# Kernel optimization log

Hardware: AMD Instinct MI355X
Metric: run time of the kernel (lower is better)

Reference implementation:

```python
import jax, jax.numpy as jnp
import numpy as np

HEADS = 12
DIM = 64
NEG = 1e12


def _rope(x, sin, cos):
    # x: [B,T,H,d]; sin/cos: [T,d] (interleaved, each freq repeated twice)
    x2 = jnp.stack([-x[..., 1::2], x[..., ::2]], axis=-1).reshape(x.shape)
    return x * cos[None, :, None, :] + x2 * sin[None, :, None, :]


def setup_inputs() -> dict:
    key = jax.random.key(0)
    k1, k2 = jax.random.split(key, 2)
    hidden_states = jax.random.normal(k1, (8, 1024, 768), dtype=jnp.float32)
    attention_mask = jnp.ones((8, 1024), dtype=jnp.int32)
    W = jax.random.normal(k2, (768, HEADS * DIM * 2), dtype=jnp.float32) * 0.02
    b = jnp.zeros((HEADS * DIM * 2,), dtype=jnp.float32)
    return {"hidden_states": hidden_states, "attention_mask": attention_mask, "W": W, "b": b}


def reference(hidden_states, attention_mask, W, b):
    B, T, D = hidden_states.shape
    H, d = HEADS, DIM
    proj = hidden_states @ W + b                      # [B,T,2*H*d]
    proj = proj.reshape(B, T, H, 2 * d)
    qw, kw = proj[..., :d], proj[..., d:]             # [B,T,H,d] each

    # sinusoidal interleaved RoPE tables
    pos = jnp.arange(T, dtype=jnp.float32)[:, None]                     # [T,1]
    inv_freq = jnp.power(10000.0, -2.0 * jnp.arange(d // 2, dtype=jnp.float32) / d)
    ang = pos * inv_freq                                                # [T,d/2]
    sin = jnp.repeat(jnp.sin(ang), 2, axis=-1)                          # [T,d]
    cos = jnp.repeat(jnp.cos(ang), 2, axis=-1)                          # [T,d]

    qw = _rope(qw, sin, cos)
    kw = _rope(kw, sin, cos)

    logits = jnp.einsum('bmhd,bnhd->bhmn', qw, kw)    # [B,H,T,T]

    # pad mask along key axis (matches torch expand of [B,1,1,T])
    m = attention_mask.astype(logits.dtype)[:, None, None, :]
    logits = logits * m - (1.0 - m) * NEG

    # strict lower-triangular mask (spans with start > end)
    tri = jnp.tril(jnp.ones((T, T), dtype=logits.dtype), -1)
    logits = logits - tri * NEG

    return logits / (d ** 0.5)
```

## Files before the change

kernel.cpp:

```cpp
#include <hip/hip_runtime.h>

#define NEG 1000000000000.0f

typedef __attribute__((ext_vector_type(4))) float f32x4;
typedef __attribute__((ext_vector_type(8))) short bf16x8;

__device__ __forceinline__ unsigned short f2bf(float f) {
    union { float f; unsigned u; } a;
    a.f = f;
    unsigned u = a.u;
    return (unsigned short)((u + 0x7FFFu + ((u >> 16) & 1u)) >> 16);
}

__device__ __forceinline__ void gload_lds16(const void* g, void* l) {
    __builtin_amdgcn_global_load_lds(
        (const __attribute__((address_space(1))) unsigned int*)g,
        (__attribute__((address_space(3))) unsigned int*)l, 16, 0, 0);
}

__global__ void cvt_bf16_kernel(const float* __restrict__ in,
                                unsigned short* __restrict__ out, int n4) {
    int i = blockIdx.x * blockDim.x + threadIdx.x;
    if (i < n4) {
        float4 v = ((const float4*)in)[i];
        ushort4 o;
        o.x = f2bf(v.x); o.y = f2bf(v.y); o.z = f2bf(v.z); o.w = f2bf(v.w);
        ((ushort4*)out)[i] = o;
    }
}

__global__ void transpose_w_kernel(const float* __restrict__ W,
                                   unsigned short* __restrict__ Wt) {
    __shared__ float tile[32][33];
    int n0 = blockIdx.x * 32, k0 = blockIdx.y * 32;
    int tx = threadIdx.x & 31, ty = threadIdx.x >> 5;
    #pragma unroll
    for (int r = 0; r < 32; r += 8)
        tile[ty + r][tx] = W[(k0 + ty + r) * 1536 + n0 + tx];
    __syncthreads();
    #pragma unroll
    for (int r = 0; r < 32; r += 8)
        Wt[(n0 + ty + r) * 768 + k0 + tx] = f2bf(tile[tx][ty + r]);
}

__global__ void rope_table_kernel(float* __restrict__ cosT, float* __restrict__ sinT) {
    int idx = blockIdx.x * blockDim.x + threadIdx.x;
    int t = idx >> 5, i = idx & 31;
    float inv = powf(10000.0f, -(float)i / 32.0f);
    float ang = (float)t * inv;
    cosT[idx] = cosf(ang);
    sinT[idx] = sinf(ang);
}

__global__ __launch_bounds__(256) void proj_rope_kernel(
    const unsigned short* __restrict__ A,
    const unsigned short* __restrict__ Bt,
    const float* __restrict__ bias,
    const float* __restrict__ cosT, const float* __restrict__ sinT,
    unsigned short* __restrict__ qout, unsigned short* __restrict__ kout)
{
    __shared__ unsigned short As[128 * 64];
    __shared__ unsigned short Bs[128 * 64];
    const int tid = threadIdx.x;
    const int lane = tid & 63, w = tid >> 6;
    const int wm = w >> 1, wn = w & 1;
    const int bm = blockIdx.y * 128, bn = blockIdx.x * 128;
    const int l15 = lane & 15, l4 = lane >> 4;

    int crow[4], gcol[4], lbase[4];
    #pragma unroll
    for (int i = 0; i < 4; ++i) {
        int c = i * 256 + w * 64 + lane;
        crow[i] = c >> 3;
        gcol[i] = ((c & 7) ^ (crow[i] & 7)) * 8;
        lbase[i] = (i * 256 + w * 64) * 8;
    }

    f32x4 acc[4][4] = {};
    const int swr = l15 & 7;

    for (int k0 = 0; k0 < 768; k0 += 64) {
        __syncthreads();
        #pragma unroll
        for (int i = 0; i < 4; ++i) {
            gload_lds16(&A[(size_t)(bm + crow[i]) * 768 + k0 + gcol[i]], &As[lbase[i]]);
            gload_lds16(&Bt[(size_t)(bn + crow[i]) * 768 + k0 + gcol[i]], &Bs[lbase[i]]);
        }
        __syncthreads();
        #pragma unroll
        for (int ks = 0; ks < 2; ++ks) {
            bf16x8 af[4], bq[4];
            #pragma unroll
            for (int i = 0; i < 4; ++i) {
                const int ar = wm * 64 + i * 16 + l15;
                const int br = wn * 64 + i * 16 + l15;
                const int cc = (ks * 4 + l4) ^ swr;
                af[i] = *(const bf16x8*)&As[(ar * 8 + cc) * 8];
                bq[i] = *(const bf16x8*)&Bs[(br * 8 + cc) * 8];
            }
            #pragma unroll
            for (int i = 0; i < 4; ++i)
                #pragma unroll
                for (int j = 0; j < 4; ++j)
                    acc[i][j] = __builtin_amdgcn_mfma_f32_16x16x32_bf16(
                        af[i], bq[j], acc[i][j], 0, 0, 0);
        }
    }

    const int rbase = bm + wm * 64 + l4 * 4;
    const int cbase = bn + wn * 64 + l15;
    #pragma unroll
    for (int mi = 0; mi < 4; ++mi) {
        #pragma unroll
        for (int ni = 0; ni < 4; ++ni) {
            const int n = cbase + ni * 16;
            const float bv = bias[n];
            const int h = n >> 7, ww = n & 127;
            const int d = ww & 63, fi = d >> 1;
            unsigned short* __restrict__ dst = (ww < 64) ? qout : kout;
            #pragma unroll
            for (int j = 0; j < 4; ++j) {
                const int m = rbase + mi * 16 + j;
                const int t = m & 1023, bb = m >> 10;
                float v = acc[mi][ni][j] + bv;
                float p = __shfl_xor(v, 1, 64);
                float c = cosT[t * 32 + fi], s = sinT[t * 32 + fi];
                float r = (d & 1) ? fmaf(v, c, p * s) : fmaf(v, c, -p * s);
                dst[((bb * 12 + h) * 1024 + t) * 64 + d] = f2bf(r);
            }
        }
    }
}

__global__ __launch_bounds__(256) void logits_kernel(
    const unsigned short* __restrict__ q, const unsigned short* __restrict__ k,
    const int* __restrict__ mask, float* __restrict__ out)
{
    const int tid = threadIdx.x;
    const int tn = blockIdx.x, tm = blockIdx.y, z = blockIdx.z;
    const int bb = z / 12;

    if (tn < tm) {
        const int c4 = (tid & 31) * 4;
        const int r0 = tid >> 5;
        const int nb = tn * 128 + c4;
        float4 v;
        #pragma unroll
        for (int e = 0; e < 4; ++e) {
            float mv = (float)mask[bb * 1024 + nb + e];
            float addc = -(1.0f - mv) * NEG;
            ((float*)&v)[e] = (addc - NEG) * 0.125f;
        }
        float* __restrict__ base = out + (size_t)(z * 1024 + tm * 128) * 1024 + nb;
        #pragma unroll
        for (int r = 0; r < 16; ++r)
            *(float4*)&base[(size_t)(r * 8 + r0) * 1024] = v;
        return;
    }

    __shared__ float tr[4][16][68];
    const int lane = tid & 63, w = tid >> 6;
    const int wm = w >> 1, wn = w & 1;
    const int l15 = lane & 15, l4 = lane >> 4;

    f32x4 acc[4][4] = {};
    const unsigned short* __restrict__ qb = q + (size_t)(z * 1024 + tm * 128) * 64;
    const unsigned short* __restrict__ kb = k + (size_t)(z * 1024 + tn * 128) * 64;

    #pragma unroll
    for (int ks = 0; ks < 2; ++ks) {
        bf16x8 af[4], bq[4];
        #pragma unroll
        for (int i = 0; i < 4; ++i) {
            af[i] = *(const bf16x8*)&qb[(size_t)(wm * 64 + i * 16 + l15) * 64 + ks * 32 + l4 * 8];
            bq[i] = *(const bf16x8*)&kb[(size_t)(wn * 64 + i * 16 + l15) * 64 + ks * 32 + l4 * 8];
        }
        #pragma unroll
        for (int i = 0; i < 4; ++i)
            #pragma unroll
            for (int j = 0; j < 4; ++j)
                acc[i][j] = __builtin_amdgcn_mfma_f32_16x16x32_bf16(
                    af[i], bq[j], acc[i][j], 0, 0, 0);
    }

    const int rw = tm * 128 + wm * 64;
    const int cw = tn * 128 + wn * 64;
    float mv[4], addc[4];
    int ncol[4];
    #pragma unroll
    for (int ni = 0; ni < 4; ++ni) {
        ncol[ni] = cw + ni * 16 + l15;
        mv[ni] = (float)mask[bb * 1024 + ncol[ni]];
        addc[ni] = -(1.0f - mv[ni]) * NEG;
    }
    float* __restrict__ outz = out + (size_t)z * 1024 * 1024;
    #pragma unroll
    for (int mi = 0; mi < 4; ++mi) {
        #pragma unroll
        for (int ni = 0; ni < 4; ++ni)
            #pragma unroll
            for (int j = 0; j < 4; ++j) {
                const int m = rw + mi * 16 + l4 * 4 + j;
                float s = acc[mi][ni][j];
                tr[w][l4 * 4 + j][ni * 16 + l15] =
                    (s * mv[ni] + addc[ni] - (ncol[ni] < m ? NEG : 0.0f)) * 0.125f;
            }
        __syncthreads();
        #pragma unroll
        for (int ri = 0; ri < 4; ++ri) {
            float4 vv = *(const float4*)&tr[w][ri * 4 + l4][l15 * 4];
            *(float4*)&outz[(size_t)(rw + mi * 16 + ri * 4 + l4) * 1024 + cw + l15 * 4] = vv;
        }
        __syncthreads();
    }
}

extern "C" void kernel_launch(void* const* d_in, const int* in_sizes, int n_in,
                              void* d_out, int out_size, void* d_ws, size_t ws_size,
                              hipStream_t stream) {
    const float* hs   = (const float*)d_in[0];
    const int*   mask = (const int*)d_in[1];
    const float* W    = (const float*)d_in[2];
    const float* bias = (const float*)d_in[3];
    float* out = (float*)d_out;

    char* ws = (char*)d_ws;
    unsigned short* qbuf = (unsigned short*)(ws + 0);
    unsigned short* kbuf = (unsigned short*)(ws + 12582912);
    unsigned short* hsb  = (unsigned short*)(ws + 25165824);
    unsigned short* wtb  = (unsigned short*)(ws + 37748736);
    float* cosT = (float*)(ws + 40108032);
    float* sinT = (float*)(ws + 40239104);

    cvt_bf16_kernel<<<6291456 / 4 / 256, 256, 0, stream>>>(hs, hsb, 6291456 / 4);
    transpose_w_kernel<<<dim3(48, 24), 256, 0, stream>>>(W, wtb);
    rope_table_kernel<<<128, 256, 0, stream>>>(cosT, sinT);
    proj_rope_kernel<<<dim3(12, 64), 256, 0, stream>>>(hsb, wtb, bias, cosT, sinT,
                                                       qbuf, kbuf);
    logits_kernel<<<dim3(8, 8, 96), 256, 0, stream>>>(qbuf, kbuf, mask, out);
}
```

Baseline: 501.4 us.

## Stage projection epilogue through LDS for vectorized RoPE stores; use wave-local fences

The projection epilogue now writes each wave's accumulator tile to a per-wave LDS buffer. It then reads rows back so each lane applies RoPE to 8 contiguous dims, using float4 cos/sin loads and a single 16-byte bf16 store, replacing the scattered 2-byte stores and shuffles. In both kernels the block-wide __syncthreads around per-wave transpose buffers is replaced by an lgkmcnt wait plus a sched barrier, since each wave only touches its own slice. This relies on wave-local LDS visibility being guaranteed by the waitcnt alone.

```diff
diff --git a/kernel.cpp b/kernel.cpp
--- a/kernel.cpp
+++ b/kernel.cpp
@@ -4,6 +4,7 @@
 
 typedef __attribute__((ext_vector_type(4))) float f32x4;
 typedef __attribute__((ext_vector_type(8))) short bf16x8;
+typedef __attribute__((ext_vector_type(8))) unsigned short u16x8;
 
 __device__ __forceinline__ unsigned short f2bf(float f) {
     union { float f; unsigned u; } a;
@@ -16,6 +17,11 @@
     __builtin_amdgcn_global_load_lds(
         (const __attribute__((address_space(1))) unsigned int*)g,
         (__attribute__((address_space(3))) unsigned int*)l, 16, 0, 0);
+}
+
+__device__ __forceinline__ void lds_fence() {
+    asm volatile("s_waitcnt lgkmcnt(0)" ::: "memory");
+    __builtin_amdgcn_sched_barrier(0);
 }
 
 __global__ void cvt_bf16_kernel(const float* __restrict__ in,
@@ -61,6 +67,7 @@
 {
     __shared__ unsigned short As[128 * 64];
     __shared__ unsigned short Bs[128 * 64];
+    __shared__ float trp[4][16][68];
     const int tid = threadIdx.x;
     const int lane = tid & 63, w = tid >> 6;
     const int wm = w >> 1, wn = w & 1;
@@ -107,28 +114,44 @@
         }
     }
 
-    const int rbase = bm + wm * 64 + l4 * 4;
-    const int cbase = bn + wn * 64 + l15;
+    const int h = blockIdx.x;
+    const int bbq = bm >> 10;
+    const int tbase = bm & 1023;
+    unsigned short* __restrict__ dstb =
+        ((wn == 0) ? qout : kout) + (size_t)(bbq * 12 + h) * 1024 * 64;
+    float bv[4];
+    #pragma unroll
+    for (int ni = 0; ni < 4; ++ni) bv[ni] = bias[bn + wn * 64 + ni * 16 + l15];
+
     #pragma unroll
     for (int mi = 0; mi < 4; ++mi) {
         #pragma unroll
-        for (int ni = 0; ni < 4; ++ni) {
-            const int n = cbase + ni * 16;
-            const float bv = bias[n];
-            const int h = n >> 7, ww = n & 127;
-            const int d = ww & 63, fi = d >> 1;
-            unsigned short* __restrict__ dst = (ww < 64) ? qout : kout;
-            #pragma unroll
-            for (int j = 0; j < 4; ++j) {
-                const int m = rbase + mi * 16 + j;
-                const int t = m & 1023, bb = m >> 10;
-                float v = acc[mi][ni][j] + bv;
-                float p = __shfl_xor(v, 1, 64);
-                float c = cosT[t * 32 + fi], s = sinT[t * 32 + fi];
-                float r = (d & 1) ? fmaf(v, c, p * s) : fmaf(v, c, -p * s);
-                dst[((bb * 12 + h) * 1024 + t) * 64 + d] = f2bf(r);
-            }
-        }
+        for (int ni = 0; ni < 4; ++ni)
+            #pragma unroll
+            for (int j = 0; j < 4; ++j)
+                trp[w][l4 * 4 + j][ni * 16 + l15] = acc[mi][ni][j] + bv[ni];
+        lds_fence();
+        #pragma unroll
+        for (int ps = 0; ps < 2; ++ps) {
+            const int tl = ps * 8 + (lane >> 3);
+            const int d0 = (lane & 7) * 8;
+            const int tg = tbase + wm * 64 + mi * 16 + tl;
+            float4 va = *(const float4*)&trp[w][tl][d0];
+            float4 vb = *(const float4*)&trp[w][tl][d0 + 4];
+            float4 cs = *(const float4*)&cosT[tg * 32 + (d0 >> 1)];
+            float4 sn = *(const float4*)&sinT[tg * 32 + (d0 >> 1)];
+            u16x8 o8;
+            o8[0] = f2bf(fmaf(va.x, cs.x, -va.y * sn.x));
+            o8[1] = f2bf(fmaf(va.y, cs.x,  va.x * sn.x));
+            o8[2] = f2bf(fmaf(va.z, cs.y, -va.w * sn.y));
+            o8[3] = f2bf(fmaf(va.w, cs.y,  va.z * sn.y));
+            o8[4] = f2bf(fmaf(vb.x, cs.z, -vb.y * sn.z));
+            o8[5] = f2bf(fmaf(vb.y, cs.z,  vb.x * sn.z));
+            o8[6] = f2bf(fmaf(vb.z, cs.w, -vb.w * sn.w));
+            o8[7] = f2bf(fmaf(vb.w, cs.w,  vb.z * sn.w));
+            *(u16x8*)&dstb[(size_t)tg * 64 + d0] = o8;
+        }
+        lds_fence();
     }
 }
 
@@ -205,13 +228,13 @@
                 tr[w][l4 * 4 + j][ni * 16 + l15] =
                     (s * mv[ni] + addc[ni] - (ncol[ni] < m ? NEG : 0.0f)) * 0.125f;
             }
-        __syncthreads();
+        lds_fence();
         #pragma unroll
         for (int ri = 0; ri < 4; ++ri) {
             float4 vv = *(const float4*)&tr[w][ri * 4 + l4][l15 * 4];
             *(float4*)&outz[(size_t)(rw + mi * 16 + ri * 4 + l4) * 1024 + cw + l15 * 4] = vv;
         }
-        __syncthreads();
+        lds_fence();
     }
 }
 
```

Result: no change. 494.3 us (-1.4%).
